# Performance work log

Measured on AMD Instinct MI355X. Metric: run time of the kernel, lower is better.

The kernel has to match this reference:

```python
import jax, jax.numpy as jnp
import numpy as np

DIM = 1024
INTER = 2048
N_EXPERTS = 8
TOP_K = 2
ROUTE_SCALE = 1.0


def setup_inputs() -> dict:
    key = jax.random.key(0)
    ks = jax.random.split(key, 4)
    x = jax.random.normal(ks[0], (4, 2048, DIM), dtype=jnp.float32)
    # Gate weight matches nn.Parameter(torch.randn(n_experts, dim))
    Wg = jax.random.normal(ks[1], (N_EXPERTS, DIM), dtype=jnp.float32)
    W1 = jax.random.normal(ks[2], (N_EXPERTS, DIM, INTER), dtype=jnp.float32) * (1.0 / np.sqrt(DIM))
    b1 = jnp.zeros((N_EXPERTS, INTER), dtype=jnp.float32)
    W2 = jax.random.normal(ks[3], (N_EXPERTS, INTER, DIM), dtype=jnp.float32) * (1.0 / np.sqrt(INTER))
    b2 = jnp.zeros((N_EXPERTS, DIM), dtype=jnp.float32)
    return {"x": x, "Wg": Wg, "W1": W1, "b1": b1, "W2": W2, "b2": b2}


def reference(x, Wg, W1, b1, W2, b2):
    # Flatten tokens: [T, D]
    xt = x.reshape(-1, DIM)
    T = xt.shape[0]

    # --- Gate: sigmoid scores, top-k, normalized weights ---
    scores = jax.nn.sigmoid(xt @ Wg.T)                       # [T, E]
    top_w, top_idx = jax.lax.top_k(scores, TOP_K)            # [T, K]
    top_w = top_w / jnp.sum(top_w, axis=-1, keepdims=True)
    top_w = top_w * ROUTE_SCALE

    # Sparse combine weights [T, E] (top_k indices are distinct per token)
    cw = jnp.zeros((T, N_EXPERTS), dtype=xt.dtype)
    cw = cw.at[jnp.arange(T)[:, None], top_idx].set(top_w)

    # --- Experts: dense per-expert MLP, weighted combine ---
    # (dropout is identity in eval mode)
    h = jax.nn.relu(jnp.einsum('td,edh->eth', xt, W1) + b1[:, None, :])   # [E, T, H]
    eo = jnp.einsum('eth,ehd->etd', h, W2) + b2[:, None, :]               # [E, T, D]
    y = jnp.einsum('etd,te->td', eo, cw)                                  # [T, D]
    return y
```

## Files before the change

### kernel.cpp

```cpp
#include <hip/hip_runtime.h>
#include <stdint.h>

#define DIM   1024
#define INTER 2048
#define NEXP  8

typedef _Float16 f16;
typedef __attribute__((ext_vector_type(4))) _Float16 f16x4;
typedef __attribute__((ext_vector_type(8))) _Float16 f16x8;
typedef __attribute__((ext_vector_type(4))) float    f32x4;

static __device__ __forceinline__ void gload16(const void* gsrc, void* lds) {
    __builtin_amdgcn_global_load_lds(
        (const __attribute__((address_space(1))) uint32_t*)gsrc,
        (__attribute__((address_space(3))) uint32_t*)lds,
        16, 0, 0);
}

__global__ void gate_convert_kernel(const float* __restrict__ x, const float* __restrict__ Wg,
                                    f16* __restrict__ xh, float* __restrict__ gw,
                                    int* __restrict__ gidx, int T) {
    const int tok  = (int)((blockIdx.x * (size_t)blockDim.x + threadIdx.x) >> 6);
    const int lane = threadIdx.x & 63;
    if (tok >= T) return;
    const float4* xr  = (const float4*)(x + (size_t)tok * DIM);
    f16*          xhr = xh + (size_t)tok * DIM;
    float s[NEXP];
    #pragma unroll
    for (int e = 0; e < NEXP; ++e) s[e] = 0.f;
    #pragma unroll
    for (int it = 0; it < 4; ++it) {
        int i = it * 64 + lane;
        float4 xv = xr[i];
        f16x4 hv = { (f16)xv.x, (f16)xv.y, (f16)xv.z, (f16)xv.w };
        *(f16x4*)(xhr + i * 4) = hv;
        #pragma unroll
        for (int e = 0; e < NEXP; ++e) {
            float4 wv = ((const float4*)(Wg + e * DIM))[i];
            s[e] += xv.x * wv.x + xv.y * wv.y + xv.z * wv.z + xv.w * wv.w;
        }
    }
    #pragma unroll
    for (int e = 0; e < NEXP; ++e) {
        #pragma unroll
        for (int off = 32; off > 0; off >>= 1) s[e] += __shfl_xor(s[e], off);
    }
    if (lane == 0) {
        float sc[NEXP];
        #pragma unroll
        for (int e = 0; e < NEXP; ++e) sc[e] = 1.f / (1.f + expf(-s[e]));
        int i0 = 0;
        #pragma unroll
        for (int e = 1; e < NEXP; ++e) if (sc[e] > sc[i0]) i0 = e;
        int i1 = -1;
        #pragma unroll
        for (int e = 0; e < NEXP; ++e) if (e != i0 && (i1 < 0 || sc[e] > sc[i1])) i1 = e;
        float w0 = sc[i0], w1 = sc[i1];
        float inv = 1.f / (w0 + w1);
        gw[2 * tok + 0] = w0 * inv;
        gw[2 * tok + 1] = w1 * inv;
        gidx[2 * tok + 0] = i0;
        gidx[2 * tok + 1] = i1;
    }
}

__global__ void transpose_conv_kernel(const float* __restrict__ W, f16* __restrict__ Wt, int K, int N) {
    __shared__ f16 tile[64][65];
    const int e  = blockIdx.z;
    const int kb = blockIdx.y * 64;
    const int nb = blockIdx.x * 64;
    const int tx = threadIdx.x & 63;
    const int ty = threadIdx.x >> 6;
    const float* We  = W  + (size_t)e * K * N;
    f16*         Wte = Wt + (size_t)e * K * N;
    #pragma unroll
    for (int i = 0; i < 16; ++i) {
        int k = ty + i * 4;
        tile[k][tx] = (f16)We[(size_t)(kb + k) * N + nb + tx];
    }
    __syncthreads();
    #pragma unroll
    for (int i = 0; i < 16; ++i) {
        int n = ty + i * 4;
        Wte[(size_t)(nb + n) * K + kb + tx] = tile[tx][n];
    }
}

__global__ __launch_bounds__(1024)
void route_kernel(const int* __restrict__ gidx, int* __restrict__ offsets,
                  int* __restrict__ tor, int* __restrict__ ros, int T) {
    const int tid  = threadIdx.x;
    const int lane = tid & 63;
    const int wv   = tid >> 6;
    const int NE   = 2 * T;
    __shared__ int wc[16][NEXP];
    __shared__ int rb[NEXP];

    int c[NEXP];
    #pragma unroll
    for (int e = 0; e < NEXP; ++e) c[e] = 0;
    for (int i = tid; i < NE; i += 1024) {
        int g = gidx[i];
        #pragma unroll
        for (int e = 0; e < NEXP; ++e) c[e] += (g == e) ? 1 : 0;
    }
    #pragma unroll
    for (int e = 0; e < NEXP; ++e) {
        #pragma unroll
        for (int off = 32; off > 0; off >>= 1) c[e] += __shfl_xor(c[e], off);
    }
    if (lane == 0) {
        #pragma unroll
        for (int e = 0; e < NEXP; ++e) wc[wv][e] = c[e];
    }
    __syncthreads();
    if (tid == 0) {
        int acc = 0;
        for (int e = 0; e < NEXP; ++e) {
            int t = 0;
            for (int w2 = 0; w2 < 16; ++w2) t += wc[w2][e];
            offsets[e] = acc;
            rb[e] = acc;
            acc += t;
        }
        offsets[NEXP] = acc;
    }
    __syncthreads();

    for (int base = 0; base < NE; base += 1024) {
        int i = base + tid;
        int g = gidx[i];
        int myrank = 0;
        #pragma unroll
        for (int e = 0; e < NEXP; ++e) {
            unsigned long long m = __ballot(g == e);
            if (g == e) myrank = __popcll(m & ((1ull << lane) - 1ull));
            if (lane == 0) wc[wv][e] = __popcll(m);
        }
        __syncthreads();
        int pre = 0;
        for (int w2 = 0; w2 < wv; ++w2) pre += wc[w2][g];
        int pos = rb[g] + pre + myrank;
        tor[pos] = i >> 1;
        ros[i]   = pos;
        __syncthreads();
        if (tid < NEXP) {
            int t = 0;
            for (int w2 = 0; w2 < 16; ++w2) t += wc[w2][tid];
            rb[tid] += t;
        }
        __syncthreads();
    }
}

template<int KD, int ND, bool RELU, bool GATHER, int RT>
__global__ __launch_bounds__(256)
void moe_gemm_kernel(const f16* __restrict__ Abase, const f16* __restrict__ Bt,
                     const float* __restrict__ bias, const int* __restrict__ offsets,
                     const int* __restrict__ tok, f16* __restrict__ Cout) {
    constexpr int NT  = ND / 128;
    constexpr int NT2 = NT / 2;
    constexpr int RT4 = RT / 4;
    const int bid = blockIdx.x;
    const int xcd = bid & 7;
    const int rtl = xcd >> 1;
    const int ntl = xcd & 1;
    const int j   = bid >> 3;
    const int nth = j % NT2;
    const int rth = (j / NT2) % RT4;
    const int e   = j / (NT2 * RT4);
    const int nt  = nth * 2 + ntl;
    const int rt  = rth * 4 + rtl;

    const int rowBeg = offsets[e];
    const int rowEnd = offsets[e + 1];
    const int row0   = rowBeg + rt * 128;
    if (row0 >= rowEnd) return;
    const int n0   = nt * 128;
    const int tid  = threadIdx.x;
    const int lane = tid & 63;
    const int wid  = tid >> 6;
    const int wr   = (wid >> 1) * 64;
    const int wc   = (wid & 1) * 64;

    __shared__ __align__(16) f16 As[3][128 * 32];
    __shared__ __align__(16) f16 Bs[3][128 * 32];

    const f16* Bte = Bt + (size_t)e * ND * KD;

    const f16* Aptr[2];
    const f16* Bptr[2];
    #pragma unroll
    for (int i = 0; i < 2; ++i) {
        int c  = i * 256 + tid;
        int r  = c >> 2;
        int kc = (c & 3) ^ ((c >> 3) & 3);
        int gr = row0 + r;
        if (gr >= rowEnd) gr = rowEnd - 1;
        int ar = GATHER ? tok[gr] : gr;
        Aptr[i] = Abase + (size_t)ar * KD + kc * 8;
        Bptr[i] = Bte + (size_t)(n0 + r) * KD + kc * 8;
    }

    auto stage = [&](int buf, int kt) {
        const int k0 = kt * 32;
        #pragma unroll
        for (int i = 0; i < 2; ++i)
            gload16(Aptr[i] + k0, &As[buf][(i * 256 + tid) * 8]);
        #pragma unroll
        for (int i = 0; i < 2; ++i)
            gload16(Bptr[i] + k0, &Bs[buf][(i * 256 + tid) * 8]);
    };

    constexpr int nK = KD / 32;
    f32x4 acc[4][4] = {};

    stage(0, 0);
    stage(1, nK > 1 ? 1 : 0);

    const int sl = ((lane >> 4) ^ ((lane >> 1) & 3)) * 8;

    int cb = 0, sbuf = 2, ktn = (2 < nK) ? 2 : nK - 1;
    for (int kt = 0; kt < nK; ++kt) {
        asm volatile("s_waitcnt vmcnt(4)" ::: "memory");
        __builtin_amdgcn_s_barrier();
        stage(sbuf, ktn);
        ktn  = (ktn + 1 < nK) ? ktn + 1 : nK - 1;
        sbuf = (sbuf == 2) ? 0 : sbuf + 1;

        const f16* Asb = As[cb];
        const f16* Bsb = Bs[cb];
        f16x8 af[4], bfr[4];
        #pragma unroll
        for (int m = 0; m < 4; ++m)
            af[m] = *(const f16x8*)&Asb[(wr + m * 16 + (lane & 15)) * 32 + sl];
        #pragma unroll
        for (int n = 0; n < 4; ++n)
            bfr[n] = *(const f16x8*)&Bsb[(wc + n * 16 + (lane & 15)) * 32 + sl];
        #pragma unroll
        for (int m = 0; m < 4; ++m)
            #pragma unroll
            for (int n = 0; n < 4; ++n)
                acc[m][n] = __builtin_amdgcn_mfma_f32_16x16x32_f16(af[m], bfr[n], acc[m][n], 0, 0, 0);
        cb = (cb == 2) ? 0 : cb + 1;
    }
    asm volatile("s_waitcnt vmcnt(0)" ::: "memory");

    const int rowsValid = rowEnd - row0;
    #pragma unroll
    for (int m = 0; m < 4; ++m) {
        #pragma unroll
        for (int n = 0; n < 4; ++n) {
            #pragma unroll
            for (int j2 = 0; j2 < 4; ++j2) {
                int rl  = wr + m * 16 + ((lane >> 4) << 2) + j2;
                int col = n0 + wc + n * 16 + (lane & 15);
                if (rl < rowsValid) {
                    float v = acc[m][n][j2] + bias[e * ND + col];
                    if (RELU) v = fmaxf(v, 0.f);
                    Cout[(size_t)(row0 + rl) * ND + col] = (f16)v;
                }
            }
        }
    }
}

__global__ void combine_kernel(const f16* __restrict__ eo, const int* __restrict__ ros,
                               const float* __restrict__ gw, float* __restrict__ y, int T) {
    int gid = blockIdx.x * 256 + threadIdx.x;
    int t   = gid >> 7;
    if (t >= T) return;
    int c0 = (gid & 127) * 8;
    int r0 = ros[2 * t], r1 = ros[2 * t + 1];
    float w0 = gw[2 * t], w1 = gw[2 * t + 1];
    f16x8 v0 = *(const f16x8*)(eo + (size_t)r0 * DIM + c0);
    f16x8 v1 = *(const f16x8*)(eo + (size_t)r1 * DIM + c0);
    f32x4 o0, o1;
    #pragma unroll
    for (int j = 0; j < 4; ++j) o0[j] = w0 * (float)v0[j] + w1 * (float)v1[j];
    #pragma unroll
    for (int j = 0; j < 4; ++j) o1[j] = w0 * (float)v0[4 + j] + w1 * (float)v1[4 + j];
    *(f32x4*)(y + (size_t)t * DIM + c0)     = o0;
    *(f32x4*)(y + (size_t)t * DIM + c0 + 4) = o1;
}

extern "C" void kernel_launch(void* const* d_in, const int* in_sizes, int n_in,
                              void* d_out, int out_size, void* d_ws, size_t ws_size,
                              hipStream_t stream) {
    const float* x  = (const float*)d_in[0];
    const float* Wg = (const float*)d_in[1];
    const float* W1 = (const float*)d_in[2];
    const float* b1 = (const float*)d_in[3];
    const float* W2 = (const float*)d_in[4];
    const float* b2 = (const float*)d_in[5];
    float* y = (float*)d_out;
    const int T = in_sizes[0] / DIM;

    char* ws = (char*)d_ws;
    size_t off = 0;
    auto alloc = [&](size_t bytes) -> char* {
        char* p = ws + off;
        off += (bytes + 255) & ~(size_t)255;
        return p;
    };
    f16* xh   = (f16*)alloc((size_t)T * DIM * 2);
    f16* w1t  = (f16*)alloc((size_t)NEXP * DIM * INTER * 2);
    f16* w2t  = (f16*)alloc((size_t)NEXP * DIM * INTER * 2);
    f16* h    = (f16*)alloc((size_t)2 * T * INTER * 2);
    f16* eo   = (f16*)alloc((size_t)2 * T * DIM * 2);
    float* gw = (float*)alloc((size_t)T * 2 * 4);
    int* gidx = (int*)alloc((size_t)T * 2 * 4);
    int* ros  = (int*)alloc((size_t)T * 2 * 4);
    int* tor  = (int*)alloc((size_t)2 * T * 4);
    int* offsets = (int*)alloc(64 * 4);

    gate_convert_kernel<<<T / 4, 256, 0, stream>>>(x, Wg, xh, gw, gidx, T);
    transpose_conv_kernel<<<dim3(INTER / 64, DIM / 64, NEXP), 256, 0, stream>>>(W1, w1t, DIM, INTER);
    transpose_conv_kernel<<<dim3(DIM / 64, INTER / 64, NEXP), 256, 0, stream>>>(W2, w2t, INTER, DIM);
    route_kernel<<<1, 1024, 0, stream>>>(gidx, offsets, tor, ros, T);
    moe_gemm_kernel<DIM, INTER, true, true, 64>
        <<<dim3((INTER / 128) * 64 * NEXP), 256, 0, stream>>>(xh, w1t, b1, offsets, tor, h);
    moe_gemm_kernel<INTER, DIM, false, false, 64>
        <<<dim3((DIM / 128) * 64 * NEXP), 256, 0, stream>>>(h, w2t, b2, offsets, tor, eo);
    combine_kernel<<<(T * DIM / 8 + 255) / 256, 256, 0, stream>>>(eo, ros, gw, y, T);
}
```

Baseline: 363.9 us.

## Enlarge MoE GEMM tiles to 256x256 with 8 waves and 4-stage pipeline

The MoE expert GEMM moves from 128x128 tiles with 4 waves to 256x256 tiles with 8 waves, each wave computing 128x64. The LDS ring buffer grows from 3 to 4 stages, with an explicit prologue and epilogue. The goal is more operand reuse per byte loaded and deeper latency hiding. In exchange the kernel uses much more LDS (128KB) and accumulator registers, which lowers occupancy, and the coarser tiles waste more work on partially filled expert row tiles.

```diff
diff --git a/kernel.cpp b/kernel.cpp
--- a/kernel.cpp
+++ b/kernel.cpp
@@ -154,11 +154,11 @@
 }
 
 template<int KD, int ND, bool RELU, bool GATHER, int RT>
-__global__ __launch_bounds__(256)
+__global__ __launch_bounds__(512)
 void moe_gemm_kernel(const f16* __restrict__ Abase, const f16* __restrict__ Bt,
                      const float* __restrict__ bias, const int* __restrict__ offsets,
                      const int* __restrict__ tok, f16* __restrict__ Cout) {
-    constexpr int NT  = ND / 128;
+    constexpr int NT  = ND / 256;
     constexpr int NT2 = NT / 2;
     constexpr int RT4 = RT / 4;
     const int bid = blockIdx.x;
@@ -174,17 +174,17 @@
 
     const int rowBeg = offsets[e];
     const int rowEnd = offsets[e + 1];
-    const int row0   = rowBeg + rt * 128;
+    const int row0   = rowBeg + rt * 256;
     if (row0 >= rowEnd) return;
-    const int n0   = nt * 128;
+    const int n0   = nt * 256;
     const int tid  = threadIdx.x;
     const int lane = tid & 63;
     const int wid  = tid >> 6;
-    const int wr   = (wid >> 1) * 64;
-    const int wc   = (wid & 1) * 64;
-
-    __shared__ __align__(16) f16 As[3][128 * 32];
-    __shared__ __align__(16) f16 Bs[3][128 * 32];
+    const int wr   = (wid >> 2) * 128;
+    const int wcn  = (wid & 3) * 64;
+
+    __shared__ __align__(16) f16 As[4][256 * 32];
+    __shared__ __align__(16) f16 Bs[4][256 * 32];
 
     const f16* Bte = Bt + (size_t)e * ND * KD;
 
@@ -192,7 +192,7 @@
     const f16* Bptr[2];
     #pragma unroll
     for (int i = 0; i < 2; ++i) {
-        int c  = i * 256 + tid;
+        int c  = i * 512 + tid;
         int r  = c >> 2;
         int kc = (c & 3) ^ ((c >> 3) & 3);
         int gr = row0 + r;
@@ -206,55 +206,64 @@
         const int k0 = kt * 32;
         #pragma unroll
         for (int i = 0; i < 2; ++i)
-            gload16(Aptr[i] + k0, &As[buf][(i * 256 + tid) * 8]);
+            gload16(Aptr[i] + k0, &As[buf][(i * 512 + tid) * 8]);
         #pragma unroll
         for (int i = 0; i < 2; ++i)
-            gload16(Bptr[i] + k0, &Bs[buf][(i * 256 + tid) * 8]);
+            gload16(Bptr[i] + k0, &Bs[buf][(i * 512 + tid) * 8]);
     };
 
-    constexpr int nK = KD / 32;
-    f32x4 acc[4][4] = {};
-
-    stage(0, 0);
-    stage(1, nK > 1 ? 1 : 0);
-
-    const int sl = ((lane >> 4) ^ ((lane >> 1) & 3)) * 8;
-
-    int cb = 0, sbuf = 2, ktn = (2 < nK) ? 2 : nK - 1;
-    for (int kt = 0; kt < nK; ++kt) {
-        asm volatile("s_waitcnt vmcnt(4)" ::: "memory");
-        __builtin_amdgcn_s_barrier();
-        stage(sbuf, ktn);
-        ktn  = (ktn + 1 < nK) ? ktn + 1 : nK - 1;
-        sbuf = (sbuf == 2) ? 0 : sbuf + 1;
-
-        const f16* Asb = As[cb];
-        const f16* Bsb = Bs[cb];
-        f16x8 af[4], bfr[4];
-        #pragma unroll
-        for (int m = 0; m < 4; ++m)
-            af[m] = *(const f16x8*)&Asb[(wr + m * 16 + (lane & 15)) * 32 + sl];
+    f32x4 acc[8][4] = {};
+
+    const int sl8 = (((lane >> 4) ^ ((lane >> 1) & 3))) * 8;
+    const int rb  = lane & 15;
+
+    auto compute = [&](int buf) {
+        const f16* Asb = As[buf];
+        const f16* Bsb = Bs[buf];
+        f16x8 bf[4];
         #pragma unroll
         for (int n = 0; n < 4; ++n)
-            bfr[n] = *(const f16x8*)&Bsb[(wc + n * 16 + (lane & 15)) * 32 + sl];
-        #pragma unroll
-        for (int m = 0; m < 4; ++m)
+            bf[n] = *(const f16x8*)&Bsb[(wcn + n * 16 + rb) * 32 + sl8];
+        #pragma unroll
+        for (int m = 0; m < 8; ++m) {
+            f16x8 af = *(const f16x8*)&Asb[(wr + m * 16 + rb) * 32 + sl8];
             #pragma unroll
             for (int n = 0; n < 4; ++n)
-                acc[m][n] = __builtin_amdgcn_mfma_f32_16x16x32_f16(af[m], bfr[n], acc[m][n], 0, 0, 0);
-        cb = (cb == 2) ? 0 : cb + 1;
-    }
+                acc[m][n] = __builtin_amdgcn_mfma_f32_16x16x32_f16(af, bf[n], acc[m][n], 0, 0, 0);
+        }
+    };
+
+    constexpr int nK = KD / 32;
+    stage(0, 0);
+    stage(1, 1);
+    stage(2, 2);
+
+    int kt = 0;
+    for (; kt < nK - 3; ++kt) {
+        asm volatile("s_waitcnt vmcnt(8)" ::: "memory");
+        __builtin_amdgcn_s_barrier();
+        stage((kt + 3) & 3, kt + 3);
+        compute(kt & 3);
+    }
+    asm volatile("s_waitcnt vmcnt(8)" ::: "memory");
+    __builtin_amdgcn_s_barrier();
+    compute(kt & 3); ++kt;
+    asm volatile("s_waitcnt vmcnt(4)" ::: "memory");
+    __builtin_amdgcn_s_barrier();
+    compute(kt & 3); ++kt;
     asm volatile("s_waitcnt vmcnt(0)" ::: "memory");
+    __builtin_amdgcn_s_barrier();
+    compute(kt & 3);
 
     const int rowsValid = rowEnd - row0;
     #pragma unroll
-    for (int m = 0; m < 4; ++m) {
+    for (int m = 0; m < 8; ++m) {
         #pragma unroll
         for (int n = 0; n < 4; ++n) {
             #pragma unroll
             for (int j2 = 0; j2 < 4; ++j2) {
                 int rl  = wr + m * 16 + ((lane >> 4) << 2) + j2;
-                int col = n0 + wc + n * 16 + (lane & 15);
+                int col = n0 + wcn + n * 16 + (lane & 15);
                 if (rl < rowsValid) {
                     float v = acc[m][n][j2] + bias[e * ND + col];
                     if (RELU) v = fmaxf(v, 0.f);
@@ -318,9 +327,9 @@
     transpose_conv_kernel<<<dim3(INTER / 64, DIM / 64, NEXP), 256, 0, stream>>>(W1, w1t, DIM, INTER);
     transpose_conv_kernel<<<dim3(DIM / 64, INTER / 64, NEXP), 256, 0, stream>>>(W2, w2t, INTER, DIM);
     route_kernel<<<1, 1024, 0, stream>>>(gidx, offsets, tor, ros, T);
-    moe_gemm_kernel<DIM, INTER, true, true, 64>
-        <<<dim3((INTER / 128) * 64 * NEXP), 256, 0, stream>>>(xh, w1t, b1, offsets, tor, h);
-    moe_gemm_kernel<INTER, DIM, false, false, 64>
-        <<<dim3((DIM / 128) * 64 * NEXP), 256, 0, stream>>>(h, w2t, b2, offsets, tor, eo);
+    moe_gemm_kernel<DIM, INTER, true, true, 32>
+        <<<dim3(((INTER / 256) / 2) * (32 / 4) * NEXP * 8), 512, 0, stream>>>(xh, w1t, b1, offsets, tor, h);
+    moe_gemm_kernel<INTER, DIM, false, false, 32>
+        <<<dim3(((DIM / 256) / 2) * (32 / 4) * NEXP * 8), 512, 0, stream>>>(h, w2t, b2, offsets, tor, eo);
     combine_kernel<<<(T * DIM / 8 + 255) / 256, 256, 0, stream>>>(eo, ros, gw, y, T);
 }
```

Result: slower. 465.1 us (+27.8%).

## Switch MoE GEMM from triple-buffered to double-buffered LDS with setprio

Applied to the files above, without the earlier changes.

Replaces the 3-stage LDS ring, which used explicit vmcnt waits and a single barrier, with a 2-stage ping-pong buffer that syncs with __syncthreads after each k-step. It also raises wave priority around the MFMA block and precomputes the LDS offsets. Grid sizes are rewritten as an equivalent expression. Halving LDS per block may raise occupancy, but the shallower prefetch and the extra barrier per iteration may expose more global-load latency.

```diff
diff --git a/kernel.cpp b/kernel.cpp
--- a/kernel.cpp
+++ b/kernel.cpp
@@ -163,14 +163,10 @@
     constexpr int RT4 = RT / 4;
     const int bid = blockIdx.x;
     const int xcd = bid & 7;
-    const int rtl = xcd >> 1;
-    const int ntl = xcd & 1;
     const int j   = bid >> 3;
-    const int nth = j % NT2;
-    const int rth = (j / NT2) % RT4;
+    const int nt  = (j % NT2) * 2 + (xcd & 1);
+    const int rt  = ((j / NT2) % RT4) * 4 + (xcd >> 1);
     const int e   = j / (NT2 * RT4);
-    const int nt  = nth * 2 + ntl;
-    const int rt  = rth * 4 + rtl;
 
     const int rowBeg = offsets[e];
     const int rowEnd = offsets[e + 1];
@@ -183,18 +179,20 @@
     const int wr   = (wid >> 1) * 64;
     const int wc   = (wid & 1) * 64;
 
-    __shared__ __align__(16) f16 As[3][128 * 32];
-    __shared__ __align__(16) f16 Bs[3][128 * 32];
+    __shared__ __align__(16) f16 As[2][128 * 32];
+    __shared__ __align__(16) f16 Bs[2][128 * 32];
 
     const f16* Bte = Bt + (size_t)e * ND * KD;
 
     const f16* Aptr[2];
     const f16* Bptr[2];
+    int ldsOff[2];
     #pragma unroll
     for (int i = 0; i < 2; ++i) {
         int c  = i * 256 + tid;
         int r  = c >> 2;
         int kc = (c & 3) ^ ((c >> 3) & 3);
+        ldsOff[i] = c * 8;
         int gr = row0 + r;
         if (gr >= rowEnd) gr = rowEnd - 1;
         int ar = GATHER ? tok[gr] : gr;
@@ -206,45 +204,45 @@
         const int k0 = kt * 32;
         #pragma unroll
         for (int i = 0; i < 2; ++i)
-            gload16(Aptr[i] + k0, &As[buf][(i * 256 + tid) * 8]);
+            gload16(Aptr[i] + k0, &As[buf][ldsOff[i]]);
         #pragma unroll
         for (int i = 0; i < 2; ++i)
-            gload16(Bptr[i] + k0, &Bs[buf][(i * 256 + tid) * 8]);
+            gload16(Bptr[i] + k0, &Bs[buf][ldsOff[i]]);
     };
 
+    f32x4 acc[4][4] = {};
+
+    const int sl = ((lane >> 4) ^ ((lane >> 1) & 3)) * 8;
+    const int rb = lane & 15;
+
     constexpr int nK = KD / 32;
-    f32x4 acc[4][4] = {};
-
     stage(0, 0);
-    stage(1, nK > 1 ? 1 : 0);
-
-    const int sl = ((lane >> 4) ^ ((lane >> 1) & 3)) * 8;
-
-    int cb = 0, sbuf = 2, ktn = (2 < nK) ? 2 : nK - 1;
+    __syncthreads();
+
+    int cur = 0;
     for (int kt = 0; kt < nK; ++kt) {
-        asm volatile("s_waitcnt vmcnt(4)" ::: "memory");
-        __builtin_amdgcn_s_barrier();
-        stage(sbuf, ktn);
-        ktn  = (ktn + 1 < nK) ? ktn + 1 : nK - 1;
-        sbuf = (sbuf == 2) ? 0 : sbuf + 1;
-
-        const f16* Asb = As[cb];
-        const f16* Bsb = Bs[cb];
+        if (kt + 1 < nK) stage(cur ^ 1, kt + 1);
+
+        const f16* Asb = As[cur];
+        const f16* Bsb = Bs[cur];
         f16x8 af[4], bfr[4];
         #pragma unroll
         for (int m = 0; m < 4; ++m)
-            af[m] = *(const f16x8*)&Asb[(wr + m * 16 + (lane & 15)) * 32 + sl];
+            af[m] = *(const f16x8*)&Asb[(wr + m * 16 + rb) * 32 + sl];
         #pragma unroll
         for (int n = 0; n < 4; ++n)
-            bfr[n] = *(const f16x8*)&Bsb[(wc + n * 16 + (lane & 15)) * 32 + sl];
+            bfr[n] = *(const f16x8*)&Bsb[(wc + n * 16 + rb) * 32 + sl];
+        __builtin_amdgcn_s_setprio(1);
         #pragma unroll
         for (int m = 0; m < 4; ++m)
             #pragma unroll
             for (int n = 0; n < 4; ++n)
                 acc[m][n] = __builtin_amdgcn_mfma_f32_16x16x32_f16(af[m], bfr[n], acc[m][n], 0, 0, 0);
-        cb = (cb == 2) ? 0 : cb + 1;
-    }
-    asm volatile("s_waitcnt vmcnt(0)" ::: "memory");
+        __builtin_amdgcn_s_setprio(0);
+
+        __syncthreads();
+        cur ^= 1;
+    }
 
     const int rowsValid = rowEnd - row0;
     #pragma unroll
@@ -319,8 +317,8 @@
     transpose_conv_kernel<<<dim3(DIM / 64, INTER / 64, NEXP), 256, 0, stream>>>(W2, w2t, INTER, DIM);
     route_kernel<<<1, 1024, 0, stream>>>(gidx, offsets, tor, ros, T);
     moe_gemm_kernel<DIM, INTER, true, true, 64>
-        <<<dim3((INTER / 128) * 64 * NEXP), 256, 0, stream>>>(xh, w1t, b1, offsets, tor, h);
+        <<<dim3(((INTER / 128) / 2) * (64 / 4) * NEXP * 8), 256, 0, stream>>>(xh, w1t, b1, offsets, tor, h);
     moe_gemm_kernel<INTER, DIM, false, false, 64>
-        <<<dim3((DIM / 128) * 64 * NEXP), 256, 0, stream>>>(h, w2t, b2, offsets, tor, eo);
+        <<<dim3(((DIM / 128) / 2) * (64 / 4) * NEXP * 8), 256, 0, stream>>>(h, w2t, b2, offsets, tor, eo);
     combine_kernel<<<(T * DIM / 8 + 255) / 256, 256, 0, stream>>>(eo, ros, gw, y, T);
 }
```

Measured after the change: 350.2 us. 1.04x faster.
